# Kernel tuning notes

Hardware: AMD Instinct MI355X
Metric: run time of the kernel (lower is better)

## Reference

```python
import jax, jax.numpy as jnp
import numpy as np

N_HEAD = 16

def setup_inputs() -> dict:
    key = jax.random.key(0)
    k1, k2, k3 = jax.random.split(key, 3)
    B, S, D = 2, 2048, 1024
    x = jax.random.normal(k1, (B, S, D), dtype=jnp.float32)
    w_attn = jax.random.normal(k2, (D, 3 * D), dtype=jnp.float32) * 0.02
    b_attn = jnp.zeros((3 * D,), dtype=jnp.float32)
    w_proj = jax.random.normal(k3, (D, D), dtype=jnp.float32) * 0.02
    b_proj = jnp.zeros((D,), dtype=jnp.float32)
    return {"x": x, "w_attn": w_attn, "b_attn": b_attn, "w_proj": w_proj, "b_proj": b_proj}

def reference(x, w_attn, b_attn, w_proj, b_proj):
    B, S, D = x.shape
    H = N_HEAD
    dh = D // H
    # c_attn: fused QKV projection
    qkv = jnp.einsum('bsd,df->bsf', x, w_attn) + b_attn  # [B,S,3D]
    q, k, v = jnp.split(qkv, 3, axis=-1)
    # split heads -> [B,H,S,dh]
    def heads(t):
        return t.reshape(B, S, H, dh).transpose(0, 2, 1, 3)
    q, k, v = heads(q), heads(k), heads(v)
    # NOTE: causal bias buffer is unused in the original forward -> non-causal attention
    scores = jnp.einsum('bhqd,bhkd->bhqk', q, k) / jnp.sqrt(jnp.float32(dh))
    probs = jax.nn.softmax(scores, axis=-1)
    out = jnp.einsum('bhqk,bhkd->bhqd', probs, v)
    # merge heads
    out = out.transpose(0, 2, 1, 3).reshape(B, S, D)
    # c_proj
    return jnp.einsum('bsd,de->bse', out, w_proj) + b_proj
```

## Files before the change

### kernel.cpp

```cpp
#include <hip/hip_runtime.h>

typedef __attribute__((ext_vector_type(8))) short short8;
typedef __attribute__((ext_vector_type(4))) float f32x4;
typedef unsigned short u16;
typedef unsigned int   u32;

#define S_  2048
#define D_  1024
#define H_  16
#define DH_ 64
#define M_  4096
#define K_  1024
#define N3_ 3072

__device__ __forceinline__ u16 f2bf(float f) {
    u32 u = __float_as_uint(f);
    u32 r = u + 0x7FFFu + ((u >> 16) & 1u);
    return (u16)(r >> 16);
}

__device__ __forceinline__ void gload_lds16(const void* g, void* l) {
    __builtin_amdgcn_global_load_lds(
        (const __attribute__((address_space(1))) u32*)g,
        (__attribute__((address_space(3))) u32*)l, 16, 0, 0);
}

__global__ __launch_bounds__(256) void convert_f32_bf16(
    const float* __restrict__ in, u16* __restrict__ out, int n4)
{
    int i = blockIdx.x * 256 + threadIdx.x;
    const int stride = gridDim.x * 256;
    for (; i < n4; i += stride) {
        float4 v = ((const float4*)in)[i];
        ushort4 o;
        o.x = f2bf(v.x); o.y = f2bf(v.y); o.z = f2bf(v.z); o.w = f2bf(v.w);
        ((ushort4*)out)[i] = o;
    }
}

__global__ __launch_bounds__(256) void transpose_f32_bf16(
    const float* __restrict__ in, u16* __restrict__ out, int rows, int cols)
{
    __shared__ float tile[32][33];
    const int tx = threadIdx.x & 31;
    const int ty = threadIdx.x >> 5;
    #pragma unroll
    for (int i = 0; i < 4; ++i) {
        int r = blockIdx.y * 32 + ty + i * 8;
        int c = blockIdx.x * 32 + tx;
        tile[ty + i * 8][tx] = in[(size_t)r * cols + c];
    }
    __syncthreads();
    #pragma unroll
    for (int i = 0; i < 4; ++i) {
        int orow = blockIdx.x * 32 + ty + i * 8;
        int ocol = blockIdx.y * 32 + tx;
        out[(size_t)orow * rows + ocol] = f2bf(tile[tx][ty + i * 8]);
    }
}

template <int EPI>
__global__ __launch_bounds__(256) void mfma_gemm(
    const u16* __restrict__ A, const u16* __restrict__ Bt,
    const float* __restrict__ bias,
    u16* __restrict__ qd, u16* __restrict__ kd, u16* __restrict__ vd,
    float* __restrict__ outp)
{
    __shared__ u16 As[128 * 32];
    __shared__ u16 Bs[128 * 32];

    const int t  = threadIdx.x;
    const int wv = t >> 6;
    const int ln = t & 63;
    const int wr = wv >> 1, wc = wv & 1;
    const int r0 = blockIdx.y * 128;
    const int c0 = blockIdx.x * 128;
    const int li = ln & 15, lq = ln >> 4;

    f32x4 acc[4][4];
    #pragma unroll
    for (int m = 0; m < 4; ++m)
        #pragma unroll
        for (int n = 0; n < 4; ++n) acc[m][n] = (f32x4){0.f, 0.f, 0.f, 0.f};

    for (int k0 = 0; k0 < K_; k0 += 32) {
        __syncthreads();
        #pragma unroll
        for (int qq = 0; qq < 2; ++qq) {
            const int slot = wv * 128 + qq * 64 + ln;
            const int row  = slot >> 2;
            const int col  = (slot & 3) * 8;
            gload_lds16(A  + (size_t)(r0 + row) * K_ + k0 + col,
                        &As[(size_t)(wv * 128 + qq * 64) * 8]);
            gload_lds16(Bt + (size_t)(c0 + row) * K_ + k0 + col,
                        &Bs[(size_t)(wv * 128 + qq * 64) * 8]);
        }
        __syncthreads();

        short8 af[4], bfr[4];
        const int qk = lq * 8;
        #pragma unroll
        for (int m = 0; m < 4; ++m)
            af[m] = *(const short8*)&As[(wr * 64 + m * 16 + li) * 32 + qk];
        #pragma unroll
        for (int n = 0; n < 4; ++n)
            bfr[n] = *(const short8*)&Bs[(wc * 64 + n * 16 + li) * 32 + qk];
        #pragma unroll
        for (int m = 0; m < 4; ++m)
            #pragma unroll
            for (int n = 0; n < 4; ++n)
                acc[m][n] = __builtin_amdgcn_mfma_f32_16x16x32_bf16(
                    af[m], bfr[n], acc[m][n], 0, 0, 0);
    }

    if (EPI == 0) {
        #pragma unroll
        for (int n = 0; n < 4; ++n) {
            const int gcol  = c0 + wc * 64 + n * 16 + li;
            const int which = gcol >> 10;
            const int rem   = gcol & 1023;
            const int h     = rem >> 6;
            const int dh    = rem & 63;
            u16* dst = (which == 0) ? qd : (which == 1) ? kd : vd;
            const float scl = (which == 0) ? 0.125f : 1.0f;
            const float bb  = bias[gcol];
            #pragma unroll
            for (int m = 0; m < 4; ++m)
                #pragma unroll
                for (int r = 0; r < 4; ++r) {
                    const int grow = r0 + wr * 64 + m * 16 + lq * 4 + r;
                    const int b = grow >> 11, s = grow & (S_ - 1);
                    dst[((size_t)(b * H_ + h) * S_ + s) * DH_ + dh] =
                        f2bf((acc[m][n][r] + bb) * scl);
                }
        }
    } else {
        #pragma unroll
        for (int n = 0; n < 4; ++n) {
            const int gcol = c0 + wc * 64 + n * 16 + li;
            const float bb = bias[gcol];
            #pragma unroll
            for (int m = 0; m < 4; ++m)
                #pragma unroll
                for (int r = 0; r < 4; ++r) {
                    const int grow = r0 + wr * 64 + m * 16 + lq * 4 + r;
                    outp[(size_t)grow * D_ + gcol] = acc[m][n][r] + bb;
                }
        }
    }
}

__global__ __launch_bounds__(256) void attn_mfma(
    const u16* __restrict__ qws, const u16* __restrict__ kws,
    const u16* __restrict__ vws, u16* __restrict__ ao)
{
    __shared__ u16 Qs[64][72];
    __shared__ u16 Ks[64][72];
    __shared__ u16 Vt[64][72];
    __shared__ u16 Ps[64][72];

    const int t  = threadIdx.x;
    const int wv = t >> 6, ln = t & 63;
    const int li = ln & 15, lq = ln >> 4;
    const int bh = blockIdx.y;
    const int q0 = blockIdx.x * 64;

    const u16* Qp = qws + (size_t)bh * S_ * DH_;
    const u16* Kp = kws + (size_t)bh * S_ * DH_;
    const u16* Vp = vws + (size_t)bh * S_ * DH_;

    #pragma unroll
    for (int i = 0; i < 2; ++i) {
        const int s = t + i * 256;
        const int row = s >> 3, c8 = (s & 7) * 8;
        *(short8*)&Qs[row][c8] = *(const short8*)(Qp + (size_t)(q0 + row) * DH_ + c8);
    }

    f32x4 o[4];
    #pragma unroll
    for (int n = 0; n < 4; ++n) o[n] = (f32x4){0.f, 0.f, 0.f, 0.f};
    float mrow[4] = {-3e38f, -3e38f, -3e38f, -3e38f};
    float lrow[4] = {0.f, 0.f, 0.f, 0.f};

    for (int kt = 0; kt < S_ / 64; ++kt) {
        const int k0 = kt * 64;
        __syncthreads();
        #pragma unroll
        for (int i = 0; i < 2; ++i) {
            const int s = t + i * 256;
            const int row = s >> 3, c8 = (s & 7) * 8;
            *(short8*)&Ks[row][c8] = *(const short8*)(Kp + (size_t)(k0 + row) * DH_ + c8);
            short8 vv = *(const short8*)(Vp + (size_t)(k0 + row) * DH_ + c8);
            #pragma unroll
            for (int j = 0; j < 8; ++j) Vt[c8 + j][row] = vv[j];
        }
        __syncthreads();

        f32x4 sacc[4];
        #pragma unroll
        for (int j = 0; j < 4; ++j) sacc[j] = (f32x4){0.f, 0.f, 0.f, 0.f};
        #pragma unroll
        for (int ks = 0; ks < 2; ++ks) {
            short8 aq = *(const short8*)&Qs[wv * 16 + li][ks * 32 + lq * 8];
            #pragma unroll
            for (int j = 0; j < 4; ++j) {
                short8 bk = *(const short8*)&Ks[j * 16 + li][ks * 32 + lq * 8];
                sacc[j] = __builtin_amdgcn_mfma_f32_16x16x32_bf16(aq, bk, sacc[j], 0, 0, 0);
            }
        }

        #pragma unroll
        for (int r = 0; r < 4; ++r) {
            float mx = fmaxf(fmaxf(sacc[0][r], sacc[1][r]), fmaxf(sacc[2][r], sacc[3][r]));
            mx = fmaxf(mx, __shfl_xor(mx, 1));
            mx = fmaxf(mx, __shfl_xor(mx, 2));
            mx = fmaxf(mx, __shfl_xor(mx, 4));
            mx = fmaxf(mx, __shfl_xor(mx, 8));
            const float mnew = fmaxf(mrow[r], mx);
            const float p0 = __expf(sacc[0][r] - mnew);
            const float p1 = __expf(sacc[1][r] - mnew);
            const float p2 = __expf(sacc[2][r] - mnew);
            const float p3 = __expf(sacc[3][r] - mnew);
            float rs = p0 + p1 + p2 + p3;
            rs += __shfl_xor(rs, 1);
            rs += __shfl_xor(rs, 2);
            rs += __shfl_xor(rs, 4);
            rs += __shfl_xor(rs, 8);
            const float scl = __expf(mrow[r] - mnew);
            lrow[r] = lrow[r] * scl + rs;
            mrow[r] = mnew;
            const int prow = wv * 16 + lq * 4 + r;
            Ps[prow][ 0 + li] = f2bf(p0);
            Ps[prow][16 + li] = f2bf(p1);
            Ps[prow][32 + li] = f2bf(p2);
            Ps[prow][48 + li] = f2bf(p3);
            #pragma unroll
            for (int n = 0; n < 4; ++n) o[n][r] *= scl;
        }

        #pragma unroll
        for (int ks = 0; ks < 2; ++ks) {
            short8 ap = *(const short8*)&Ps[wv * 16 + li][ks * 32 + lq * 8];
            #pragma unroll
            for (int n = 0; n < 4; ++n) {
                short8 bv = *(const short8*)&Vt[n * 16 + li][ks * 32 + lq * 8];
                o[n] = __builtin_amdgcn_mfma_f32_16x16x32_bf16(ap, bv, o[n], 0, 0, 0);
            }
        }
    }

    const int b = bh >> 4, h = bh & 15;
    #pragma unroll
    for (int r = 0; r < 4; ++r) {
        const float inv = 1.0f / lrow[r];
        const int s = q0 + wv * 16 + lq * 4 + r;
        #pragma unroll
        for (int n = 0; n < 4; ++n) {
            const int col = h * 64 + n * 16 + li;
            ao[((size_t)b * S_ + s) * D_ + col] = f2bf(o[n][r] * inv);
        }
    }
}

extern "C" void kernel_launch(void* const* d_in, const int* in_sizes, int n_in,
                              void* d_out, int out_size, void* d_ws, size_t ws_size,
                              hipStream_t stream)
{
    const float* x      = (const float*)d_in[0];
    const float* w_attn = (const float*)d_in[1];
    const float* b_attn = (const float*)d_in[2];
    const float* w_proj = (const float*)d_in[3];
    const float* b_proj = (const float*)d_in[4];
    float* out = (float*)d_out;

    char* ws = (char*)d_ws;
    u16* x_bf = (u16*)(ws);
    u16* wat  = (u16*)(ws + 8388608);
    u16* wpj  = (u16*)(ws + 14680064);
    u16* qws  = (u16*)(ws + 16777216);
    u16* kws  = (u16*)(ws + 25165824);
    u16* vws  = (u16*)(ws + 33554432);
    u16* ao   = (u16*)(ws + 41943040);

    convert_f32_bf16<<<1024, 256, 0, stream>>>(x, x_bf, M_ * K_ / 4);
    transpose_f32_bf16<<<dim3(N3_ / 32, K_ / 32), 256, 0, stream>>>(w_attn, wat, K_, N3_);
    transpose_f32_bf16<<<dim3(D_ / 32, K_ / 32), 256, 0, stream>>>(w_proj, wpj, K_, D_);

    mfma_gemm<0><<<dim3(N3_ / 128, M_ / 128), 256, 0, stream>>>(
        x_bf, wat, b_attn, qws, kws, vws, nullptr);

    attn_mfma<<<dim3(S_ / 64, 32), 256, 0, stream>>>(qws, kws, vws, ao);

    mfma_gemm<1><<<dim3(D_ / 128, M_ / 128), 256, 0, stream>>>(
        ao, wpj, b_proj, nullptr, nullptr, nullptr, out);
}
```

Before: 311.0 us.

## Write V pre-transposed from QKV GEMM, swizzle LDS, keep Q in registers

The QKV GEMM epilogue now writes V in a [b,h,dh,s] transposed layout, so the attention kernel can load V^T tiles with vector loads instead of doing a scalar transpose into LDS. The K, V^T and P tiles in LDS use an XOR swizzle in place of padding to avoid bank conflicts. Q fragments are held in registers rather than staged through LDS, and MFMA sections are wrapped in setprio with a launch-bounds occupancy hint. The risk is that the transposed V write in the GEMM epilogue becomes strided (stride S along rows), which may slow that kernel.

```diff
diff --git a/kernel.cpp b/kernel.cpp
--- a/kernel.cpp
+++ b/kernel.cpp
@@ -121,7 +121,6 @@
             const int rem   = gcol & 1023;
             const int h     = rem >> 6;
             const int dh    = rem & 63;
-            u16* dst = (which == 0) ? qd : (which == 1) ? kd : vd;
             const float scl = (which == 0) ? 0.125f : 1.0f;
             const float bb  = bias[gcol];
             #pragma unroll
@@ -130,8 +129,13 @@
                 for (int r = 0; r < 4; ++r) {
                     const int grow = r0 + wr * 64 + m * 16 + lq * 4 + r;
                     const int b = grow >> 11, s = grow & (S_ - 1);
-                    dst[((size_t)(b * H_ + h) * S_ + s) * DH_ + dh] =
-                        f2bf((acc[m][n][r] + bb) * scl);
+                    const u16 val = f2bf((acc[m][n][r] + bb) * scl);
+                    if (which == 2) {
+                        vd[((size_t)(b * H_ + h) * DH_ + dh) * S_ + s] = val;
+                    } else {
+                        u16* dst = (which == 0) ? qd : kd;
+                        dst[((size_t)(b * H_ + h) * S_ + s) * DH_ + dh] = val;
+                    }
                 }
         }
     } else {
@@ -150,14 +154,13 @@
     }
 }
 
-__global__ __launch_bounds__(256) void attn_mfma(
+__global__ __launch_bounds__(256, 4) void attn_mfma(
     const u16* __restrict__ qws, const u16* __restrict__ kws,
-    const u16* __restrict__ vws, u16* __restrict__ ao)
-{
-    __shared__ u16 Qs[64][72];
-    __shared__ u16 Ks[64][72];
-    __shared__ u16 Vt[64][72];
-    __shared__ u16 Ps[64][72];
+    const u16* __restrict__ vtws, u16* __restrict__ ao)
+{
+    __shared__ u16 Ks[64 * 64];
+    __shared__ u16 Vt[64 * 64];
+    __shared__ u16 Ps[64 * 64];
 
     const int t  = threadIdx.x;
     const int wv = t >> 6, ln = t & 63;
@@ -165,15 +168,14 @@
     const int bh = blockIdx.y;
     const int q0 = blockIdx.x * 64;
 
-    const u16* Qp = qws + (size_t)bh * S_ * DH_;
-    const u16* Kp = kws + (size_t)bh * S_ * DH_;
-    const u16* Vp = vws + (size_t)bh * S_ * DH_;
-
-    #pragma unroll
-    for (int i = 0; i < 2; ++i) {
-        const int s = t + i * 256;
-        const int row = s >> 3, c8 = (s & 7) * 8;
-        *(short8*)&Qs[row][c8] = *(const short8*)(Qp + (size_t)(q0 + row) * DH_ + c8);
+    const u16* Kp  = kws  + (size_t)bh * S_ * DH_;
+    const u16* Vtp = vtws + (size_t)bh * DH_ * S_;
+
+    short8 aq[2];
+    {
+        const u16* Qp = qws + ((size_t)bh * S_ + q0 + wv * 16 + li) * DH_ + lq * 8;
+        aq[0] = *(const short8*)(Qp);
+        aq[1] = *(const short8*)(Qp + 32);
     }
 
     f32x4 o[4];
@@ -187,27 +189,32 @@
         __syncthreads();
         #pragma unroll
         for (int i = 0; i < 2; ++i) {
-            const int s = t + i * 256;
-            const int row = s >> 3, c8 = (s & 7) * 8;
-            *(short8*)&Ks[row][c8] = *(const short8*)(Kp + (size_t)(k0 + row) * DH_ + c8);
-            short8 vv = *(const short8*)(Vp + (size_t)(k0 + row) * DH_ + c8);
-            #pragma unroll
-            for (int j = 0; j < 8; ++j) Vt[c8 + j][row] = vv[j];
+            const int s   = t + i * 256;
+            const int row = s >> 3;
+            const int c16 = s & 7;
+            const int off = (row * 128 + c16 * 16) ^ ((row & 7) << 4);
+            *(short8*)((char*)Ks + off) =
+                *(const short8*)(Kp + (size_t)(k0 + row) * DH_ + c16 * 8);
+            *(short8*)((char*)Vt + off) =
+                *(const short8*)(Vtp + (size_t)row * S_ + k0 + c16 * 8);
         }
         __syncthreads();
 
         f32x4 sacc[4];
         #pragma unroll
         for (int j = 0; j < 4; ++j) sacc[j] = (f32x4){0.f, 0.f, 0.f, 0.f};
+        __builtin_amdgcn_s_setprio(1);
         #pragma unroll
         for (int ks = 0; ks < 2; ++ks) {
-            short8 aq = *(const short8*)&Qs[wv * 16 + li][ks * 32 + lq * 8];
             #pragma unroll
             for (int j = 0; j < 4; ++j) {
-                short8 bk = *(const short8*)&Ks[j * 16 + li][ks * 32 + lq * 8];
-                sacc[j] = __builtin_amdgcn_mfma_f32_16x16x32_bf16(aq, bk, sacc[j], 0, 0, 0);
+                const int rrow = j * 16 + li;
+                const int roff = (rrow * 128 + ks * 64 + lq * 16) ^ ((li & 7) << 4);
+                short8 bk = *(const short8*)((char*)Ks + roff);
+                sacc[j] = __builtin_amdgcn_mfma_f32_16x16x32_bf16(aq[ks], bk, sacc[j], 0, 0, 0);
             }
         }
+        __builtin_amdgcn_s_setprio(0);
 
         #pragma unroll
         for (int r = 0; r < 4; ++r) {
@@ -230,23 +237,31 @@
             lrow[r] = lrow[r] * scl + rs;
             mrow[r] = mnew;
             const int prow = wv * 16 + lq * 4 + r;
-            Ps[prow][ 0 + li] = f2bf(p0);
-            Ps[prow][16 + li] = f2bf(p1);
-            Ps[prow][32 + li] = f2bf(p2);
-            Ps[prow][48 + li] = f2bf(p3);
+            const int pbase = prow * 128;
+            const int psw   = (prow & 7) << 4;
+            *(u16*)((char*)Ps + ((pbase + (     li) * 2) ^ psw)) = f2bf(p0);
+            *(u16*)((char*)Ps + ((pbase + (16 + li) * 2) ^ psw)) = f2bf(p1);
+            *(u16*)((char*)Ps + ((pbase + (32 + li) * 2) ^ psw)) = f2bf(p2);
+            *(u16*)((char*)Ps + ((pbase + (48 + li) * 2) ^ psw)) = f2bf(p3);
             #pragma unroll
             for (int n = 0; n < 4; ++n) o[n][r] *= scl;
         }
 
+        __builtin_amdgcn_s_setprio(1);
         #pragma unroll
         for (int ks = 0; ks < 2; ++ks) {
-            short8 ap = *(const short8*)&Ps[wv * 16 + li][ks * 32 + lq * 8];
+            const int arow = wv * 16 + li;
+            const int aoff = (arow * 128 + ks * 64 + lq * 16) ^ ((li & 7) << 4);
+            short8 ap = *(const short8*)((char*)Ps + aoff);
             #pragma unroll
             for (int n = 0; n < 4; ++n) {
-                short8 bv = *(const short8*)&Vt[n * 16 + li][ks * 32 + lq * 8];
+                const int vrow = n * 16 + li;
+                const int voff = (vrow * 128 + ks * 64 + lq * 16) ^ ((li & 7) << 4);
+                short8 bv = *(const short8*)((char*)Vt + voff);
                 o[n] = __builtin_amdgcn_mfma_f32_16x16x32_bf16(ap, bv, o[n], 0, 0, 0);
             }
         }
+        __builtin_amdgcn_s_setprio(0);
     }
 
     const int b = bh >> 4, h = bh & 15;
@@ -279,7 +294,7 @@
     u16* wpj  = (u16*)(ws + 14680064);
     u16* qws  = (u16*)(ws + 16777216);
     u16* kws  = (u16*)(ws + 25165824);
-    u16* vws  = (u16*)(ws + 33554432);
+    u16* vtws = (u16*)(ws + 33554432);
     u16* ao   = (u16*)(ws + 41943040);
 
     convert_f32_bf16<<<1024, 256, 0, stream>>>(x, x_bf, M_ * K_ / 4);
@@ -287,9 +302,9 @@
     transpose_f32_bf16<<<dim3(D_ / 32, K_ / 32), 256, 0, stream>>>(w_proj, wpj, K_, D_);
 
     mfma_gemm<0><<<dim3(N3_ / 128, M_ / 128), 256, 0, stream>>>(
-        x_bf, wat, b_attn, qws, kws, vws, nullptr);
-
-    attn_mfma<<<dim3(S_ / 64, 32), 256, 0, stream>>>(qws, kws, vws, ao);
+        x_bf, wat, b_attn, qws, kws, vtws, nullptr);
+
+    attn_mfma<<<dim3(S_ / 64, 32), 256, 0, stream>>>(qws, kws, vtws, ao);
 
     mfma_gemm<1><<<dim3(D_ / 128, M_ / 128), 256, 0, stream>>>(
         ao, wpj, b_proj, nullptr, nullptr, nullptr, out);
```

Measured after the change: 253.4 us. 18.5% less time.
